# Performance work log

Measured on AMD Instinct MI355X. Metric: run time of the kernel, lower is better.

Reference implementation:

```python
import jax, jax.numpy as jnp
import numpy as np

N, DIN, D, H, L, S, E = 3072, 64, 128, 4, 2, 4, 49152
NEG = -2.0**32 + 1.0


def _layernorm(x, g, b, eps=1e-5):
    m = jnp.mean(x, axis=-1, keepdims=True)
    v = jnp.var(x, axis=-1, keepdims=True)
    return (x - m) * jax.lax.rsqrt(v + eps) * g + b


def setup_inputs() -> dict:
    key = jax.random.key(0)
    ks = jax.random.split(key, 24)
    w = lambda k, shp: (0.02 * jax.random.normal(k, shp)).astype(jnp.float32)
    inp = {
        "x": jax.random.normal(ks[0], (N, DIN), dtype=jnp.float32),
        "edge_index": jax.random.randint(ks[1], (2, E), 0, N, dtype=jnp.int64) if jax.config.jax_enable_x64 else jax.random.randint(ks[1], (2, E), 0, N).astype(jnp.int32),
        "shortest_path_len": jax.random.randint(ks[2], (N, N), 0, 11).astype(jnp.int32),
        "edge_feat": jax.random.normal(ks[3], (N, N, S), dtype=jnp.float32),
        # input projection
        "node_W": w(ks[4], (DIN, D)), "node_b": jnp.zeros((D,), jnp.float32),
        # centrality / spatial / edge encodings
        "deg_emb": w(ks[5], (N, D)),
        "sp_emb": w(ks[6], (11, 1)),
        "edge_W": w(ks[7], (S, S)), "edge_b": jnp.zeros((S,), jnp.float32),
        # per-layer stacked attention params
        "ln1_g": jnp.ones((L, D), jnp.float32), "ln1_b": jnp.zeros((L, D), jnp.float32),
        "Wq": w(ks[8], (L, H, D, D)), "bq": jnp.zeros((L, H, D), jnp.float32),
        "Wk": w(ks[9], (L, H, D, D)), "bk": jnp.zeros((L, H, D), jnp.float32),
        "Wv": w(ks[10], (L, H, D, D)), "bv": jnp.zeros((L, H, D), jnp.float32),
        "Wo": w(ks[11], (L, H * D, D)), "bo": jnp.zeros((L, D), jnp.float32),
        "ln2_g": jnp.ones((L, D), jnp.float32), "ln2_b": jnp.zeros((L, D), jnp.float32),
        "ff_W": w(ks[12], (L, D, D)), "ff_b": jnp.zeros((L, D), jnp.float32),
        # output projection
        "out_W": w(ks[13], (D, D)), "out_b": jnp.zeros((D,), jnp.float32),
    }
    return inp


def reference(x, edge_index, shortest_path_len, edge_feat,
              node_W, node_b, deg_emb, sp_emb, edge_W, edge_b,
              ln1_g, ln1_b, Wq, bq, Wk, bk, Wv, bv, Wo, bo,
              ln2_g, ln2_b, ff_W, ff_b, out_W, out_b):
    # padding mask from raw features
    mask_idx = (jnp.sum(x, axis=1) != 0).astype(x.dtype)            # [N]
    mask = mask_idx[:, None] * mask_idx[None, :]                    # [N,N]

    h = x @ node_W + node_b                                         # [N,D]
    # centrality: degree of edge destinations
    deg = jax.ops.segment_sum(jnp.ones((edge_index.shape[1],), jnp.int32),
                              edge_index[1], num_segments=N)        # [N]
    h = h + deg_emb[deg]

    spatial = sp_emb[shortest_path_len][..., 0]                     # [N,N]
    edge_m = (edge_feat @ edge_W + edge_b).mean(axis=-1)            # [N,N]
    bias = spatial + edge_m
    scale = 1.0 / jnp.sqrt(jnp.asarray(D, x.dtype))

    for l in range(L):
        x_ln = _layernorm(h, ln1_g[l], ln1_b[l])                    # [N,D]
        q = jnp.einsum('nd,hdk->hnk', x_ln, Wq[l]) + bq[l][:, None, :]
        k = jnp.einsum('nd,hdk->hnk', x_ln, Wk[l]) + bk[l][:, None, :]
        v = jnp.einsum('nd,hdk->hnk', x_ln, Wv[l]) + bv[l][:, None, :]
        a = jnp.einsum('hnk,hmk->hnm', q, k) * scale + bias[None]   # [H,N,N]
        a = jnp.where(mask[None] == 0, NEG, a)
        s = jax.nn.softmax(a, axis=-1)
        s = jnp.where(mask[None] == 0, 0.0, s)
        o = jnp.einsum('hnm,hmd->hnd', s, v)                        # [H,N,D]
        cat = jnp.transpose(o, (1, 0, 2)).reshape(N, H * D)         # [N,H*D]
        x_out = cat @ Wo[l] + bo[l] + h
        h = _layernorm(x_out, ln2_g[l], ln2_b[l]) @ ff_W[l] + ff_b[l] + x_out

    return h @ out_W + out_b
```

## Files before the change

### kernel.cpp

```cpp
#include <hip/hip_runtime.h>
#include <math.h>

static constexpr int N   = 3072;
static constexpr int DIN = 64;
static constexpr int D   = 128;
static constexpr int H   = 4;
static constexpr int E   = 49152;
#define NEGV  (-4294967295.0f)
#define SCALE (0.08838834764831845f)

typedef unsigned short u16;
typedef __attribute__((ext_vector_type(8))) short short8;
typedef __attribute__((ext_vector_type(4))) float f32x4;
typedef __attribute__((ext_vector_type(4))) unsigned short u16x4;

__device__ __forceinline__ u16 f2bf(float f){
  unsigned int u = __float_as_uint(f);
  u += 0x7fff + ((u >> 16) & 1);
  return (u16)(u >> 16);
}
__device__ __forceinline__ float bf2f(u16 u){
  return __uint_as_float(((unsigned int)u) << 16);
}

__global__ void k_zero_deg(int* __restrict__ deg){
  int i = blockIdx.x*blockDim.x + threadIdx.x;
  if(i < N) deg[i] = 0;
}

__global__ void k_deg(const int* __restrict__ ei, int* __restrict__ deg){
  int e = blockIdx.x*blockDim.x + threadIdx.x;
  if(e < E) atomicAdd(&deg[ei[E + e]], 1);
}

__global__ void k_h0(const float* __restrict__ x, const float* __restrict__ nodeW,
                     const float* __restrict__ nodeb, const float* __restrict__ degemb,
                     const int* __restrict__ deg, float* __restrict__ mask,
                     float* __restrict__ h){
  const int i = blockIdx.x, t = threadIdx.x;
  float xv = x[i*DIN + t];
  float s = xv;
  #pragma unroll
  for(int o=32;o;o>>=1) s += __shfl_xor(s, o);
  if(t == 0) mask[i] = (s != 0.0f) ? 1.0f : 0.0f;
  __shared__ float xr[DIN];
  xr[t] = xv;
  __syncthreads();
  int dg = deg[i]; dg = dg > N-1 ? N-1 : dg;
  float a0 = nodeb[t]      + degemb[dg*D + t];
  float a1 = nodeb[t + 64] + degemb[dg*D + t + 64];
  #pragma unroll
  for(int u=0; u<DIN; ++u){
    float xu = xr[u];
    a0 = fmaf(xu, nodeW[u*D + t],      a0);
    a1 = fmaf(xu, nodeW[u*D + t + 64], a1);
  }
  h[i*D + t]      = a0;
  h[i*D + t + 64] = a1;
}

__global__ void k_bias(const int* __restrict__ spl, const float* __restrict__ ef,
                       const float* __restrict__ spe, const float* __restrict__ eW,
                       const float* __restrict__ eb, const float* __restrict__ mask,
                       u16* __restrict__ biasm){
  int idx = blockIdx.x*blockDim.x + threadIdx.x;
  int i = idx / N, j = idx % N;
  float wm0 = (eW[0] + eW[1] + eW[2] + eW[3])  * 0.25f;
  float wm1 = (eW[4] + eW[5] + eW[6] + eW[7])  * 0.25f;
  float wm2 = (eW[8] + eW[9] + eW[10]+ eW[11]) * 0.25f;
  float wm3 = (eW[12]+ eW[13]+ eW[14]+ eW[15]) * 0.25f;
  float bm  = (eb[0] + eb[1] + eb[2] + eb[3])  * 0.25f;
  float4 e4 = reinterpret_cast<const float4*>(ef)[idx];
  float em = fmaf(e4.x, wm0, fmaf(e4.y, wm1, fmaf(e4.z, wm2, fmaf(e4.w, wm3, bm))));
  float b = spe[spl[idx]] + em;
  float mk = mask[i]*mask[j];
  biasm[idx] = f2bf((mk != 0.0f) ? b : NEGV);
}

__global__ void k_ln(const float* __restrict__ in, const float* __restrict__ g,
                     const float* __restrict__ b, float* __restrict__ out){
  const int w = threadIdx.x >> 6, lane = threadIdx.x & 63;
  const int row = blockIdx.x*4 + w;
  const float* r = in + row*D;
  float v0 = r[lane], v1 = r[lane + 64];
  float s = v0 + v1, sq = v0*v0 + v1*v1;
  #pragma unroll
  for(int o=32;o;o>>=1){ s += __shfl_xor(s, o); sq += __shfl_xor(sq, o); }
  float mean = s*(1.0f/128.0f);
  float var  = sq*(1.0f/128.0f) - mean*mean;
  float inv  = rsqrtf(var + 1e-5f);
  out[row*D + lane]      = (v0 - mean)*inv*g[lane]      + b[lane];
  out[row*D + lane + 64] = (v1 - mean)*inv*g[lane + 64] + b[lane + 64];
}

__global__ __launch_bounds__(256) void k_wt_all(const float* __restrict__ Wq, const float* __restrict__ Wk,
    const float* __restrict__ Wv, const float* __restrict__ ffW, const float* __restrict__ outW,
    u16* __restrict__ wt_qkv, u16* __restrict__ wt_ff, u16* __restrict__ wt_out){
  __shared__ float t[32][33];
  const int z = blockIdx.y;
  const float* src; u16* dst;
  if(z < 24){
    int l = z/12, r = z%12;
    const float* W = (r>>2)==0 ? Wq : (r>>2)==1 ? Wk : Wv;
    src = W + (size_t)(l*4 + (r&3))*16384;
    dst = wt_qkv + (size_t)z*16384;
  } else if(z < 26){
    src = ffW + (size_t)(z-24)*16384; dst = wt_ff + (size_t)(z-24)*16384;
  } else { src = outW; dst = wt_out; }
  const int ki = blockIdx.x & 3, ni = blockIdx.x >> 2;
  const int tid = threadIdx.x;
  #pragma unroll
  for(int i=0;i<4;i++){
    int idx = tid + i*256, r = idx>>5, c = idx&31;
    t[r][c] = src[(size_t)(ki*32+r)*128 + ni*32 + c];
  }
  __syncthreads();
  #pragma unroll
  for(int i=0;i<4;i++){
    int idx = tid + i*256, r = idx>>5, c = idx&31;
    dst[(size_t)(ni*32+r)*128 + ki*32 + c] = f2bf(t[c][r]);
  }
}

__global__ __launch_bounds__(256) void k_wt_wo(const float* __restrict__ Wo, u16* __restrict__ wt_wo){
  __shared__ float t[32][33];
  const int l = blockIdx.y;
  const float* src = Wo + (size_t)l*65536;
  u16* dst = wt_wo + (size_t)l*65536;
  const int ki = blockIdx.x & 15, ni = blockIdx.x >> 4;
  const int tid = threadIdx.x;
  #pragma unroll
  for(int i=0;i<4;i++){
    int idx = tid + i*256, r = idx>>5, c = idx&31;
    t[r][c] = src[(size_t)(ki*32+r)*128 + ni*32 + c];
  }
  __syncthreads();
  #pragma unroll
  for(int i=0;i<4;i++){
    int idx = tid + i*256, r = idx>>5, c = idx&31;
    dst[(size_t)(ni*32+r)*512 + ki*32 + c] = f2bf(t[c][r]);
  }
}

template<int K, bool RES, bool BF16OUT>
__device__ __forceinline__ void mgemm_body(const float* __restrict__ A, const u16* __restrict__ Bt,
                                           const float* __restrict__ bias, const float* __restrict__ res,
                                           void* __restrict__ Cv){
  __shared__ u16 As[64*128];
  __shared__ u16 Bs[128*128];
  const int tid = threadIdx.x, w = tid>>6, lane = tid&63;
  const int g4 = lane>>4, l16 = lane&15;
  const int m0 = blockIdx.x*64;
  const int srow = tid>>4, sch = tid&15;
  f32x4 acc[8];
  #pragma unroll
  for(int nt=0;nt<8;++nt) acc[nt] = (f32x4){0.f,0.f,0.f,0.f};
  for(int k0 = 0; k0 < K; k0 += 128){
    __syncthreads();
    #pragma unroll
    for(int it=0;it<4;++it){
      int row = it*16 + srow;
      const float4* ap = reinterpret_cast<const float4*>(A + (size_t)(m0+row)*K + k0 + sch*8);
      float4 x0 = ap[0], x1 = ap[1];
      u16x4 p0, p1;
      p0.x=f2bf(x0.x); p0.y=f2bf(x0.y); p0.z=f2bf(x0.z); p0.w=f2bf(x0.w);
      p1.x=f2bf(x1.x); p1.y=f2bf(x1.y); p1.z=f2bf(x1.z); p1.w=f2bf(x1.w);
      u16* dst = &As[row*128 + ((sch ^ (row&15))*8)];
      *reinterpret_cast<u16x4*>(dst)     = p0;
      *reinterpret_cast<u16x4*>(dst + 4) = p1;
    }
    #pragma unroll
    for(int it=0;it<8;++it){
      int row = it*16 + srow;
      short8 b = *reinterpret_cast<const short8*>(Bt + (size_t)row*K + k0 + sch*8);
      *reinterpret_cast<short8*>(&Bs[row*128 + ((sch ^ (row&15))*8)]) = b;
    }
    __syncthreads();
    __builtin_amdgcn_s_setprio(1);
    #pragma unroll
    for(int c=0;c<4;++c){
      short8 af = *reinterpret_cast<const short8*>(&As[(w*16+l16)*128 + (((c*4+g4) ^ l16)*8)]);
      #pragma unroll
      for(int nt=0;nt<8;++nt){
        short8 bf = *reinterpret_cast<const short8*>(&Bs[(nt*16+l16)*128 + (((c*4+g4) ^ l16)*8)]);
        acc[nt] = __builtin_amdgcn_mfma_f32_16x16x32_bf16(af, bf, acc[nt], 0, 0, 0);
      }
    }
    __builtin_amdgcn_s_setprio(0);
  }
  const int mrow = m0 + w*16 + g4*4;
  #pragma unroll
  for(int nt=0;nt<8;++nt){
    const int col = nt*16 + l16;
    float bi = bias[col];
    #pragma unroll
    for(int rg=0;rg<4;++rg){
      float v = acc[nt][rg] + bi;
      if(RES) v += res[(size_t)(mrow+rg)*128 + col];
      if(BF16OUT) ((u16*)Cv)[(size_t)(mrow+rg)*128 + col] = f2bf(v);
      else        ((float*)Cv)[(size_t)(mrow+rg)*128 + col] = v;
    }
  }
}

__global__ __launch_bounds__(256) void k_mqkv(const float* __restrict__ xln, const u16* __restrict__ wt_qkv,
    const float* __restrict__ bq, const float* __restrict__ bk, const float* __restrict__ bv,
    u16* __restrict__ q, u16* __restrict__ k, u16* __restrict__ v, int l){
  const int z = blockIdx.y, which = z>>2, head = z&3;
  const u16* Bt = wt_qkv + (size_t)(l*12 + z)*16384;
  const float* bb = (which==0 ? bq : which==1 ? bk : bv) + (l*H + head)*D;
  u16* out = (which==0 ? q : which==1 ? k : v) + (size_t)head*N*D;
  mgemm_body<128,false,true>(xln, Bt, bb, nullptr, out);
}

__global__ __launch_bounds__(256) void k_mwo(const float* __restrict__ ocat, const u16* __restrict__ wt_wo,
    const float* __restrict__ bo, const float* __restrict__ hres, float* __restrict__ xout, int l){
  mgemm_body<512,true,false>(ocat, wt_wo + (size_t)l*65536, bo + l*D, hres, xout);
}

__global__ __launch_bounds__(256) void k_mff(const float* __restrict__ xln, const u16* __restrict__ wt_ff,
    const float* __restrict__ ffb, const float* __restrict__ xout, float* __restrict__ h, int l){
  mgemm_body<128,true,false>(xln, wt_ff + (size_t)l*16384, ffb + l*D, xout, h);
}

__global__ __launch_bounds__(256) void k_mout(const float* __restrict__ h, const u16* __restrict__ wt_out,
    const float* __restrict__ outb, float* __restrict__ out){
  mgemm_body<128,false,false>(h, wt_out, outb, nullptr, out);
}

__global__ __launch_bounds__(256) void k_vt(const u16* __restrict__ vb, u16* __restrict__ vT){
  __shared__ u16 t[32][33];
  const int n0 = blockIdx.x*32, d0 = blockIdx.y*32, head = blockIdx.z;
  const int tid = threadIdx.x;
  #pragma unroll
  for(int i=0;i<4;i++){
    int idx = tid + i*256, r = idx >> 5, c = idx & 31;
    t[r][c] = vb[((size_t)head*N + n0 + r)*D + d0 + c];
  }
  __syncthreads();
  #pragma unroll
  for(int i=0;i<4;i++){
    int idx = tid + i*256, r = idx >> 5, c = idx & 31;
    vT[((size_t)head*D + d0 + r)*N + n0 + c] = t[c][r];
  }
}

__global__ __launch_bounds__(256) void k_attn(const u16* __restrict__ q, const u16* __restrict__ k,
                     const u16* __restrict__ vT, const u16* __restrict__ biasm,
                     float* __restrict__ opart, float* __restrict__ mpart, float* __restrict__ lpart,
                     int kvlen){
  const int tid  = threadIdx.x;
  const int w    = tid >> 6;
  const int lane = tid & 63;
  const int g4 = lane >> 4, l16 = lane & 15;
  const int head = blockIdx.y, sp = blockIdx.z;
  const int r0 = blockIdx.x*64 + w*16;
  __shared__ u16 Ks[64*128];
  __shared__ u16 Vs[64*128];
  __shared__ u16 P[4][16][40];

  const u16* qbase = q + ((size_t)head*N + r0)*D;
  short8 qf[4];
  #pragma unroll
  for(int c=0;c<4;c++)
    qf[c] = *reinterpret_cast<const short8*>(qbase + l16*D + c*32 + g4*8);

  f32x4 o[8];
  #pragma unroll
  for(int dt=0;dt<8;dt++) o[dt] = (f32x4){0.f,0.f,0.f,0.f};
  float m = -INFINITY, lsum = 0.0f;

  const u16* kh   = k  + (size_t)head*N*D;
  const u16* vTh  = vT + (size_t)head*D*N;
  const u16* brow = biasm + (size_t)(r0 + l16)*N;
  const int kv0 = sp*kvlen;

  const int krow = tid >> 4, kch = tid & 15;
  const int vrow = tid >> 3, vch = tid & 7;

  for(int j0 = kv0; j0 < kv0 + kvlen; j0 += 64){
    short8 kreg[4], vreg[4];
    #pragma unroll
    for(int it=0; it<4; ++it)
      kreg[it] = *reinterpret_cast<const short8*>(kh + (size_t)(j0 + it*16 + krow)*D + kch*8);
    #pragma unroll
    for(int it=0; it<4; ++it)
      vreg[it] = *reinterpret_cast<const short8*>(vTh + (size_t)(it*32 + vrow)*N + j0 + vch*8);
    u16x4 bb[4];
    #pragma unroll
    for(int z=0; z<4; ++z)
      bb[z] = *reinterpret_cast<const u16x4*>(brow + j0 + z*16 + g4*4);

    __syncthreads();
    #pragma unroll
    for(int it=0; it<4; ++it){
      int row = it*16 + krow;
      *reinterpret_cast<short8*>(&Ks[row*128 + ((kch ^ (row&15))*8)]) = kreg[it];
    }
    #pragma unroll
    for(int it=0; it<4; ++it){
      int d = it*32 + vrow;
      int row = d & 63, ch = ((d>>6)<<3) | vch;
      *reinterpret_cast<short8*>(&Vs[row*128 + ((ch ^ (row&15))*8)]) = vreg[it];
    }
    __syncthreads();

    #pragma unroll
    for(int ks=0; ks<2; ++ks){
      short8 kf[8];
      const int rowA = ks*32 + l16, rowB = rowA + 16;
      #pragma unroll
      for(int c=0;c<4;c++){
        kf[c]   = *reinterpret_cast<const short8*>(&Ks[rowA*128 + (((c*4+g4) ^ l16)*8)]);
        kf[4+c] = *reinterpret_cast<const short8*>(&Ks[rowB*128 + (((c*4+g4) ^ l16)*8)]);
      }
      f32x4 sA = (f32x4){0.f,0.f,0.f,0.f}, sB = sA;
      __builtin_amdgcn_s_setprio(1);
      #pragma unroll
      for(int c=0;c<4;c++){
        sA = __builtin_amdgcn_mfma_f32_16x16x32_bf16(kf[c],   qf[c], sA, 0, 0, 0);
        sB = __builtin_amdgcn_mfma_f32_16x16x32_bf16(kf[4+c], qf[c], sB, 0, 0, 0);
      }
      __builtin_amdgcn_s_setprio(0);
      u16x4 bA = bb[2*ks], bB = bb[2*ks+1];
      sA[0] = fmaf(sA[0], SCALE, bf2f(bA.x)); sA[1] = fmaf(sA[1], SCALE, bf2f(bA.y));
      sA[2] = fmaf(sA[2], SCALE, bf2f(bA.z)); sA[3] = fmaf(sA[3], SCALE, bf2f(bA.w));
      sB[0] = fmaf(sB[0], SCALE, bf2f(bB.x)); sB[1] = fmaf(sB[1], SCALE, bf2f(bB.y));
      sB[2] = fmaf(sB[2], SCALE, bf2f(bB.z)); sB[3] = fmaf(sB[3], SCALE, bf2f(bB.w));
      float pmax = fmaxf(fmaxf(fmaxf(sA[0],sA[1]), fmaxf(sA[2],sA[3])),
                         fmaxf(fmaxf(sB[0],sB[1]), fmaxf(sB[2],sB[3])));
      pmax = fmaxf(pmax, __shfl_xor(pmax, 16));
      pmax = fmaxf(pmax, __shfl_xor(pmax, 32));
      if(!__all(pmax - m <= 8.0f)){
        float mnew = fmaxf(m, pmax);
        float corr = __expf(m - mnew);
        lsum *= corr;
        float c0 = __shfl(corr, (lane & 48) | (g4*4 + 0));
        float c1 = __shfl(corr, (lane & 48) | (g4*4 + 1));
        float c2 = __shfl(corr, (lane & 48) | (g4*4 + 2));
        float c3 = __shfl(corr, (lane & 48) | (g4*4 + 3));
        #pragma unroll
        for(int dt=0;dt<8;dt++){
          o[dt][0] *= c0; o[dt][1] *= c1; o[dt][2] *= c2; o[dt][3] *= c3;
        }
        m = mnew;
      }
      f32x4 pA, pB;
      #pragma unroll
      for(int rg=0;rg<4;rg++){ pA[rg] = __expf(sA[rg] - m); pB[rg] = __expf(sB[rg] - m); }
      float ps = (pA[0]+pA[1]) + (pA[2]+pA[3]) + ((pB[0]+pB[1]) + (pB[2]+pB[3]));
      ps += __shfl_xor(ps, 16);
      ps += __shfl_xor(ps, 32);
      lsum += ps;
      u16x4 wa, wb;
      wa.x = f2bf(pA[0]); wa.y = f2bf(pA[1]); wa.z = f2bf(pA[2]); wa.w = f2bf(pA[3]);
      wb.x = f2bf(pB[0]); wb.y = f2bf(pB[1]); wb.z = f2bf(pB[2]); wb.w = f2bf(pB[3]);
      *reinterpret_cast<u16x4*>(&P[w][l16][g4*4])      = wa;
      *reinterpret_cast<u16x4*>(&P[w][l16][16 + g4*4]) = wb;
      short8 pf = *reinterpret_cast<const short8*>(&P[w][l16][g4*8]);
      __builtin_amdgcn_s_setprio(1);
      #pragma unroll
      for(int dt=0;dt<8;dt++){
        int d = dt*16 + l16;
        int row = d & 63;
        int ch  = ((dt>>2)<<3) | (ks<<2) | g4;
        short8 vf = *reinterpret_cast<const short8*>(&Vs[row*128 + ((ch ^ l16)*8)]);
        o[dt] = __builtin_amdgcn_mfma_f32_16x16x32_bf16(pf, vf, o[dt], 0, 0, 0);
      }
      __builtin_amdgcn_s_setprio(0);
    }
  }

  float* ob = opart + ((size_t)((sp*H + head)*N) + r0)*D;
  #pragma unroll
  for(int dt=0;dt<8;dt++){
    #pragma unroll
    for(int rg=0;rg<4;rg++)
      ob[(size_t)(g4*4+rg)*D + dt*16 + l16] = o[dt][rg];
  }
  if(g4 == 0){
    mpart[(size_t)(sp*H + head)*N + r0 + l16] = m;
    lpart[(size_t)(sp*H + head)*N + r0 + l16] = lsum;
  }
}

template<int S>
__global__ __launch_bounds__(256) void k_comb(const float* __restrict__ opart,
                      const float* __restrict__ mpart, const float* __restrict__ lpart,
                      const float* __restrict__ mask, float* __restrict__ ocat){
  int idx = blockIdx.x*256 + threadIdx.x;
  int d = idx & (D-1);
  int r = (idx >> 7) % N;
  int h = idx / (N*D);
  float mv[S], lv[S];
  float M = -INFINITY;
  #pragma unroll
  for(int s=0;s<S;s++){
    size_t p = (size_t)(s*H + h)*N + r;
    mv[s] = mpart[p]; lv[s] = lpart[p];
    M = fmaxf(M, mv[s]);
  }
  float denom = 0.f, val = 0.f;
  #pragma unroll
  for(int s=0;s<S;s++){
    size_t p = (size_t)(s*H + h)*N + r;
    float wgt = __expf(mv[s] - M);
    denom = fmaf(lv[s], wgt, denom);
    val   = fmaf(opart[p*D + d], wgt, val);
  }
  ocat[(size_t)r*(H*D) + h*D + d] = val * (mask[r] / denom);
}

extern "C" void kernel_launch(void* const* d_in, const int* in_sizes, int n_in,
                              void* d_out, int out_size, void* d_ws, size_t ws_size,
                              hipStream_t stream){
  const float* x      = (const float*)d_in[0];
  const int*   ei     = (const int*)  d_in[1];
  const int*   spl    = (const int*)  d_in[2];
  const float* ef     = (const float*)d_in[3];
  const float* nodeW  = (const float*)d_in[4];
  const float* nodeb  = (const float*)d_in[5];
  const float* degemb = (const float*)d_in[6];
  const float* spe    = (const float*)d_in[7];
  const float* eW     = (const float*)d_in[8];
  const float* eb     = (const float*)d_in[9];
  const float* ln1g   = (const float*)d_in[10];
  const float* ln1b   = (const float*)d_in[11];
  const float* Wq     = (const float*)d_in[12];
  const float* bq     = (const float*)d_in[13];
  const float* Wk     = (const float*)d_in[14];
  const float* bk     = (const float*)d_in[15];
  const float* Wv     = (const float*)d_in[16];
  const float* bv     = (const float*)d_in[17];
  const float* Wo     = (const float*)d_in[18];
  const float* bo     = (const float*)d_in[19];
  const float* ln2g   = (const float*)d_in[20];
  const float* ln2b   = (const float*)d_in[21];
  const float* ffW    = (const float*)d_in[22];
  const float* ffb    = (const float*)d_in[23];
  const float* outW   = (const float*)d_in[24];
  const float* outb   = (const float*)d_in[25];

  constexpr size_t WT_ELEMS = 24*16384 + 2*16384 + 16384 + 2*65536;
  auto needed = [](int s)->size_t{
    size_t fl = 8192 + 3*(size_t)N*D + (size_t)N*H*D;
    size_t bf = 4*(size_t)H*N*D + (size_t)N*N;
    size_t pf = (size_t)s*H*N*D + 2*(size_t)s*H*N;
    return fl*4 + bf*2 + pf*4 + WT_ELEMS*2;
  };
  int S = 2;
  if(needed(4) <= ws_size) S = 4;

  float* ws   = (float*)d_ws;
  int*   deg  = (int*)ws;
  float* mask = ws + 4096;
  float* h    = ws + 8192;
  float* xln  = h    + N*D;
  float* xout = xln  + N*D;
  float* ocat = xout + N*D;
  u16*   qb   = (u16*)(ocat + N*H*D);
  u16*   kb   = qb + (size_t)H*N*D;
  u16*   vb   = kb + (size_t)H*N*D;
  u16*   vT   = vb + (size_t)H*N*D;
  u16*   biasm= vT + (size_t)H*N*D;
  float* opart= (float*)(biasm + (size_t)N*N);
  float* mpart= opart + (size_t)S*H*N*D;
  float* lpart= mpart + (size_t)S*H*N;
  u16*   wt_qkv = (u16*)(lpart + (size_t)S*H*N);
  u16*   wt_ff  = wt_qkv + 24*16384;
  u16*   wt_out = wt_ff  + 2*16384;
  u16*   wt_wo  = wt_out + 16384;

  k_wt_all<<<dim3(16, 27), 256, 0, stream>>>(Wq, Wk, Wv, ffW, outW, wt_qkv, wt_ff, wt_out);
  k_wt_wo<<<dim3(64, 2), 256, 0, stream>>>(Wo, wt_wo);
  k_zero_deg<<<(N+255)/256, 256, 0, stream>>>(deg);
  k_deg<<<(E+255)/256, 256, 0, stream>>>(ei, deg);
  k_h0<<<N, 64, 0, stream>>>(x, nodeW, nodeb, degemb, deg, mask, h);
  k_bias<<<(N*N)/256, 256, 0, stream>>>(spl, ef, spe, eW, eb, mask, biasm);

  for(int l = 0; l < 2; ++l){
    k_ln<<<N/4, 256, 0, stream>>>(h, ln1g + l*D, ln1b + l*D, xln);
    k_mqkv<<<dim3(N/64, 12), 256, 0, stream>>>(xln, wt_qkv, bq, bk, bv, qb, kb, vb, l);
    k_vt<<<dim3(N/32, D/32, H), 256, 0, stream>>>(vb, vT);
    k_attn<<<dim3(N/64, H, S), 256, 0, stream>>>(qb, kb, vT, biasm, opart, mpart, lpart, N/S);
    if(S == 4) k_comb<4><<<(H*N*D)/256, 256, 0, stream>>>(opart, mpart, lpart, mask, ocat);
    else       k_comb<2><<<(H*N*D)/256, 256, 0, stream>>>(opart, mpart, lpart, mask, ocat);
    k_mwo<<<N/64, 256, 0, stream>>>(ocat, wt_wo, bo, h, xout, l);
    k_ln<<<N/4, 256, 0, stream>>>(xout, ln2g + l*D, ln2b + l*D, xln);
    k_mff<<<N/64, 256, 0, stream>>>(xln, wt_ff, ffb, xout, h, l);
  }
  k_mout<<<N/64, 256, 0, stream>>>(h, wt_out, outb, (float*)d_out);
}
```

Baseline: 236.5 us.

## Fuse layernorms, split-softmax combine and V transpose into neighboring GEMMs; prefetch attention tiles

```diff
diff --git a/kernel.cpp b/kernel.cpp
--- a/kernel.cpp
+++ b/kernel.cpp
@@ -35,8 +35,9 @@
 
 __global__ void k_h0(const float* __restrict__ x, const float* __restrict__ nodeW,
                      const float* __restrict__ nodeb, const float* __restrict__ degemb,
-                     const int* __restrict__ deg, float* __restrict__ mask,
-                     float* __restrict__ h){
+                     const int* __restrict__ deg, const float* __restrict__ g1,
+                     const float* __restrict__ b1, float* __restrict__ mask,
+                     float* __restrict__ h, float* __restrict__ xln){
   const int i = blockIdx.x, t = threadIdx.x;
   float xv = x[i*DIN + t];
   float s = xv;
@@ -57,6 +58,14 @@
   }
   h[i*D + t]      = a0;
   h[i*D + t + 64] = a1;
+  float s2 = a0 + a1, sq = a0*a0 + a1*a1;
+  #pragma unroll
+  for(int o=32;o;o>>=1){ s2 += __shfl_xor(s2, o); sq += __shfl_xor(sq, o); }
+  float mean = s2*(1.0f/128.0f);
+  float var  = sq*(1.0f/128.0f) - mean*mean;
+  float inv  = rsqrtf(var + 1e-5f);
+  xln[i*D + t]      = (a0 - mean)*inv*g1[t]      + b1[t];
+  xln[i*D + t + 64] = (a1 - mean)*inv*g1[t + 64] + b1[t + 64];
 }
 
 __global__ void k_bias(const int* __restrict__ spl, const float* __restrict__ ef,
@@ -77,22 +86,6 @@
   biasm[idx] = f2bf((mk != 0.0f) ? b : NEGV);
 }
 
-__global__ void k_ln(const float* __restrict__ in, const float* __restrict__ g,
-                     const float* __restrict__ b, float* __restrict__ out){
-  const int w = threadIdx.x >> 6, lane = threadIdx.x & 63;
-  const int row = blockIdx.x*4 + w;
-  const float* r = in + row*D;
-  float v0 = r[lane], v1 = r[lane + 64];
-  float s = v0 + v1, sq = v0*v0 + v1*v1;
-  #pragma unroll
-  for(int o=32;o;o>>=1){ s += __shfl_xor(s, o); sq += __shfl_xor(sq, o); }
-  float mean = s*(1.0f/128.0f);
-  float var  = sq*(1.0f/128.0f) - mean*mean;
-  float inv  = rsqrtf(var + 1e-5f);
-  out[row*D + lane]      = (v0 - mean)*inv*g[lane]      + b[lane];
-  out[row*D + lane + 64] = (v1 - mean)*inv*g[lane + 64] + b[lane + 64];
-}
-
 __global__ __launch_bounds__(256) void k_wt_all(const float* __restrict__ Wq, const float* __restrict__ Wk,
     const float* __restrict__ Wv, const float* __restrict__ ffW, const float* __restrict__ outW,
     u16* __restrict__ wt_qkv, u16* __restrict__ wt_ff, u16* __restrict__ wt_out){
@@ -142,10 +135,9 @@
   }
 }
 
-template<int K, bool RES, bool BF16OUT>
+template<int MODE>
 __device__ __forceinline__ void mgemm_body(const float* __restrict__ A, const u16* __restrict__ Bt,
-                                           const float* __restrict__ bias, const float* __restrict__ res,
-                                           void* __restrict__ Cv){
+                                           const float* __restrict__ bias, void* __restrict__ Cv){
   __shared__ u16 As[64*128];
   __shared__ u16 Bs[128*128];
   const int tid = threadIdx.x, w = tid>>6, lane = tid&63;
@@ -155,16 +147,120 @@
   f32x4 acc[8];
   #pragma unroll
   for(int nt=0;nt<8;++nt) acc[nt] = (f32x4){0.f,0.f,0.f,0.f};
-  for(int k0 = 0; k0 < K; k0 += 128){
+  #pragma unroll
+  for(int it=0;it<4;++it){
+    int row = it*16 + srow;
+    const float4* ap = reinterpret_cast<const float4*>(A + (size_t)(m0+row)*128 + sch*8);
+    float4 x0 = ap[0], x1 = ap[1];
+    u16x4 p0, p1;
+    p0.x=f2bf(x0.x); p0.y=f2bf(x0.y); p0.z=f2bf(x0.z); p0.w=f2bf(x0.w);
+    p1.x=f2bf(x1.x); p1.y=f2bf(x1.y); p1.z=f2bf(x1.z); p1.w=f2bf(x1.w);
+    u16* dst = &As[row*128 + ((sch ^ (row&15))*8)];
+    *reinterpret_cast<u16x4*>(dst)     = p0;
+    *reinterpret_cast<u16x4*>(dst + 4) = p1;
+  }
+  #pragma unroll
+  for(int it=0;it<8;++it){
+    int row = it*16 + srow;
+    short8 b = *reinterpret_cast<const short8*>(Bt + (size_t)row*128 + sch*8);
+    *reinterpret_cast<short8*>(&Bs[row*128 + ((sch ^ (row&15))*8)]) = b;
+  }
+  __syncthreads();
+  __builtin_amdgcn_s_setprio(1);
+  #pragma unroll
+  for(int c=0;c<4;++c){
+    short8 af = *reinterpret_cast<const short8*>(&As[(w*16+l16)*128 + (((c*4+g4) ^ l16)*8)]);
+    #pragma unroll
+    for(int nt=0;nt<8;++nt){
+      short8 bf = *reinterpret_cast<const short8*>(&Bs[(nt*16+l16)*128 + (((c*4+g4) ^ l16)*8)]);
+      acc[nt] = __builtin_amdgcn_mfma_f32_16x16x32_bf16(af, bf, acc[nt], 0, 0, 0);
+    }
+  }
+  __builtin_amdgcn_s_setprio(0);
+  const int mrow = m0 + w*16 + g4*4;
+  #pragma unroll
+  for(int nt=0;nt<8;++nt){
+    const int col = nt*16 + l16;
+    float bi = bias[col];
+    if(MODE == 2){
+      u16x4 t;
+      t.x = f2bf(acc[nt][0] + bi); t.y = f2bf(acc[nt][1] + bi);
+      t.z = f2bf(acc[nt][2] + bi); t.w = f2bf(acc[nt][3] + bi);
+      *reinterpret_cast<u16x4*>((u16*)Cv + (size_t)col*N + mrow) = t;
+    } else {
+      #pragma unroll
+      for(int rg=0;rg<4;++rg){
+        float v = acc[nt][rg] + bi;
+        if(MODE == 1) ((u16*)Cv)[(size_t)(mrow+rg)*128 + col] = f2bf(v);
+        else          ((float*)Cv)[(size_t)(mrow+rg)*128 + col] = v;
+      }
+    }
+  }
+}
+
+__global__ __launch_bounds__(256) void k_mqkv(const float* __restrict__ xln, const u16* __restrict__ wt_qkv,
+    const float* __restrict__ bq, const float* __restrict__ bk, const float* __restrict__ bv,
+    u16* __restrict__ q, u16* __restrict__ k, u16* __restrict__ vT, int l){
+  const int z = blockIdx.y, which = z>>2, head = z&3;
+  const u16* Bt = wt_qkv + (size_t)(l*12 + z)*16384;
+  if(which == 0)      mgemm_body<1>(xln, Bt, bq + (l*H+head)*D, q  + (size_t)head*N*D);
+  else if(which == 1) mgemm_body<1>(xln, Bt, bk + (l*H+head)*D, k  + (size_t)head*N*D);
+  else                mgemm_body<2>(xln, Bt, bv + (l*H+head)*D, vT + (size_t)head*N*D);
+}
+
+__global__ __launch_bounds__(256) void k_mout(const float* __restrict__ h, const u16* __restrict__ wt_out,
+    const float* __restrict__ outb, float* __restrict__ out){
+  mgemm_body<0>(h, wt_out, outb, out);
+}
+
+template<int S>
+__global__ __launch_bounds__(256) void k_mwo(const float* __restrict__ opart, const float* __restrict__ mpart,
+    const float* __restrict__ lpart, const float* __restrict__ mask, const u16* __restrict__ wt,
+    const float* __restrict__ bo, const float* __restrict__ hres,
+    float* __restrict__ xout, float* __restrict__ xln,
+    const float* __restrict__ g2, const float* __restrict__ b2){
+  __shared__ u16 As[64*128];
+  __shared__ u16 Bs[128*128];
+  const int tid = threadIdx.x, w = tid>>6, lane = tid&63;
+  const int g4 = lane>>4, l16 = lane&15;
+  const int m0 = blockIdx.x*64;
+  const int srow = tid>>4, sch = tid&15;
+  f32x4 acc[8];
+  #pragma unroll
+  for(int nt=0;nt<8;++nt) acc[nt] = (f32x4){0.f,0.f,0.f,0.f};
+  for(int k0 = 0; k0 < 512; k0 += 128){
+    const int hh = k0 >> 7;
     __syncthreads();
     #pragma unroll
     for(int it=0;it<4;++it){
       int row = it*16 + srow;
-      const float4* ap = reinterpret_cast<const float4*>(A + (size_t)(m0+row)*K + k0 + sch*8);
-      float4 x0 = ap[0], x1 = ap[1];
+      int grow = m0 + row;
+      float w_[S]; float M = -INFINITY; float mv[S], lv[S];
+      #pragma unroll
+      for(int s=0;s<S;++s){
+        mv[s] = mpart[(size_t)(s*H + hh)*N + grow];
+        lv[s] = lpart[(size_t)(s*H + hh)*N + grow];
+        M = fmaxf(M, mv[s]);
+      }
+      float denom = 0.f;
+      #pragma unroll
+      for(int s=0;s<S;++s){ w_[s] = __expf(mv[s] - M); denom = fmaf(lv[s], w_[s], denom); }
+      float scale = mask[grow] / denom;
+      const int d = sch*8;
+      float4 v0 = make_float4(0,0,0,0), v1 = make_float4(0,0,0,0);
+      #pragma unroll
+      for(int s=0;s<S;++s){
+        const float4* op = reinterpret_cast<const float4*>(
+            opart + ((size_t)(s*H + hh)*N + grow)*D + d);
+        float4 a = op[0], b = op[1];
+        v0.x = fmaf(a.x, w_[s], v0.x); v0.y = fmaf(a.y, w_[s], v0.y);
+        v0.z = fmaf(a.z, w_[s], v0.z); v0.w = fmaf(a.w, w_[s], v0.w);
+        v1.x = fmaf(b.x, w_[s], v1.x); v1.y = fmaf(b.y, w_[s], v1.y);
+        v1.z = fmaf(b.z, w_[s], v1.z); v1.w = fmaf(b.w, w_[s], v1.w);
+      }
       u16x4 p0, p1;
-      p0.x=f2bf(x0.x); p0.y=f2bf(x0.y); p0.z=f2bf(x0.z); p0.w=f2bf(x0.w);
-      p1.x=f2bf(x1.x); p1.y=f2bf(x1.y); p1.z=f2bf(x1.z); p1.w=f2bf(x1.w);
+      p0.x=f2bf(v0.x*scale); p0.y=f2bf(v0.y*scale); p0.z=f2bf(v0.z*scale); p0.w=f2bf(v0.w*scale);
+      p1.x=f2bf(v1.x*scale); p1.y=f2bf(v1.y*scale); p1.z=f2bf(v1.z*scale); p1.w=f2bf(v1.w*scale);
       u16* dst = &As[row*128 + ((sch ^ (row&15))*8)];
       *reinterpret_cast<u16x4*>(dst)     = p0;
       *reinterpret_cast<u16x4*>(dst + 4) = p1;
@@ -172,7 +268,7 @@
     #pragma unroll
     for(int it=0;it<8;++it){
       int row = it*16 + srow;
-      short8 b = *reinterpret_cast<const short8*>(Bt + (size_t)row*K + k0 + sch*8);
+      short8 b = *reinterpret_cast<const short8*>(wt + (size_t)row*512 + k0 + sch*8);
       *reinterpret_cast<short8*>(&Bs[row*128 + ((sch ^ (row&15))*8)]) = b;
     }
     __syncthreads();
@@ -189,59 +285,127 @@
     __builtin_amdgcn_s_setprio(0);
   }
   const int mrow = m0 + w*16 + g4*4;
+  float s_[4] = {0,0,0,0}, q_[4] = {0,0,0,0};
   #pragma unroll
   for(int nt=0;nt<8;++nt){
     const int col = nt*16 + l16;
-    float bi = bias[col];
+    float bi = bo[col];
     #pragma unroll
     for(int rg=0;rg<4;++rg){
-      float v = acc[nt][rg] + bi;
-      if(RES) v += res[(size_t)(mrow+rg)*128 + col];
-      if(BF16OUT) ((u16*)Cv)[(size_t)(mrow+rg)*128 + col] = f2bf(v);
-      else        ((float*)Cv)[(size_t)(mrow+rg)*128 + col] = v;
-    }
-  }
-}
-
-__global__ __launch_bounds__(256) void k_mqkv(const float* __restrict__ xln, const u16* __restrict__ wt_qkv,
-    const float* __restrict__ bq, const float* __restrict__ bk, const float* __restrict__ bv,
-    u16* __restrict__ q, u16* __restrict__ k, u16* __restrict__ v, int l){
-  const int z = blockIdx.y, which = z>>2, head = z&3;
-  const u16* Bt = wt_qkv + (size_t)(l*12 + z)*16384;
-  const float* bb = (which==0 ? bq : which==1 ? bk : bv) + (l*H + head)*D;
-  u16* out = (which==0 ? q : which==1 ? k : v) + (size_t)head*N*D;
-  mgemm_body<128,false,true>(xln, Bt, bb, nullptr, out);
-}
-
-__global__ __launch_bounds__(256) void k_mwo(const float* __restrict__ ocat, const u16* __restrict__ wt_wo,
-    const float* __restrict__ bo, const float* __restrict__ hres, float* __restrict__ xout, int l){
-  mgemm_body<512,true,false>(ocat, wt_wo + (size_t)l*65536, bo + l*D, hres, xout);
-}
-
-__global__ __launch_bounds__(256) void k_mff(const float* __restrict__ xln, const u16* __restrict__ wt_ff,
-    const float* __restrict__ ffb, const float* __restrict__ xout, float* __restrict__ h, int l){
-  mgemm_body<128,true,false>(xln, wt_ff + (size_t)l*16384, ffb + l*D, xout, h);
-}
-
-__global__ __launch_bounds__(256) void k_mout(const float* __restrict__ h, const u16* __restrict__ wt_out,
-    const float* __restrict__ outb, float* __restrict__ out){
-  mgemm_body<128,false,false>(h, wt_out, outb, nullptr, out);
-}
-
-__global__ __launch_bounds__(256) void k_vt(const u16* __restrict__ vb, u16* __restrict__ vT){
-  __shared__ u16 t[32][33];
-  const int n0 = blockIdx.x*32, d0 = blockIdx.y*32, head = blockIdx.z;
-  const int tid = threadIdx.x;
-  #pragma unroll
-  for(int i=0;i<4;i++){
-    int idx = tid + i*256, r = idx >> 5, c = idx & 31;
-    t[r][c] = vb[((size_t)head*N + n0 + r)*D + d0 + c];
+      float v = acc[nt][rg] + bi + hres[(size_t)(mrow+rg)*128 + col];
+      acc[nt][rg] = v;
+      s_[rg] += v; q_[rg] = fmaf(v, v, q_[rg]);
+    }
+  }
+  #pragma unroll
+  for(int o=1;o<16;o<<=1){
+    #pragma unroll
+    for(int rg=0;rg<4;++rg){ s_[rg] += __shfl_xor(s_[rg], o); q_[rg] += __shfl_xor(q_[rg], o); }
+  }
+  float mean[4], inv[4];
+  #pragma unroll
+  for(int rg=0;rg<4;++rg){
+    mean[rg] = s_[rg]*(1.0f/128.0f);
+    float var = q_[rg]*(1.0f/128.0f) - mean[rg]*mean[rg];
+    inv[rg] = rsqrtf(var + 1e-5f);
+  }
+  #pragma unroll
+  for(int nt=0;nt<8;++nt){
+    const int col = nt*16 + l16;
+    float gg = g2[col], bb = b2[col];
+    #pragma unroll
+    for(int rg=0;rg<4;++rg){
+      float v = acc[nt][rg];
+      xout[(size_t)(mrow+rg)*128 + col] = v;
+      xln [(size_t)(mrow+rg)*128 + col] = (v - mean[rg])*inv[rg]*gg + bb;
+    }
+  }
+}
+
+__global__ __launch_bounds__(256) void k_mff(const float* __restrict__ xlnin, const u16* __restrict__ wt,
+    const float* __restrict__ ffb, const float* __restrict__ res, float* __restrict__ hout,
+    float* __restrict__ xlnout, const float* __restrict__ g1n, const float* __restrict__ b1n,
+    int write_ln){
+  __shared__ u16 As[64*128];
+  __shared__ u16 Bs[128*128];
+  const int tid = threadIdx.x, w = tid>>6, lane = tid&63;
+  const int g4 = lane>>4, l16 = lane&15;
+  const int m0 = blockIdx.x*64;
+  const int srow = tid>>4, sch = tid&15;
+  f32x4 acc[8];
+  #pragma unroll
+  for(int nt=0;nt<8;++nt) acc[nt] = (f32x4){0.f,0.f,0.f,0.f};
+  #pragma unroll
+  for(int it=0;it<4;++it){
+    int row = it*16 + srow;
+    const float4* ap = reinterpret_cast<const float4*>(xlnin + (size_t)(m0+row)*128 + sch*8);
+    float4 x0 = ap[0], x1 = ap[1];
+    u16x4 p0, p1;
+    p0.x=f2bf(x0.x); p0.y=f2bf(x0.y); p0.z=f2bf(x0.z); p0.w=f2bf(x0.w);
+    p1.x=f2bf(x1.x); p1.y=f2bf(x1.y); p1.z=f2bf(x1.z); p1.w=f2bf(x1.w);
+    u16* dst = &As[row*128 + ((sch ^ (row&15))*8)];
+    *reinterpret_cast<u16x4*>(dst)     = p0;
+    *reinterpret_cast<u16x4*>(dst + 4) = p1;
+  }
+  #pragma unroll
+  for(int it=0;it<8;++it){
+    int row = it*16 + srow;
+    short8 b = *reinterpret_cast<const short8*>(wt + (size_t)row*128 + sch*8);
+    *reinterpret_cast<short8*>(&Bs[row*128 + ((sch ^ (row&15))*8)]) = b;
   }
   __syncthreads();
-  #pragma unroll
-  for(int i=0;i<4;i++){
-    int idx = tid + i*256, r = idx >> 5, c = idx & 31;
-    vT[((size_t)head*D + d0 + r)*N + n0 + c] = t[c][r];
+  __builtin_amdgcn_s_setprio(1);
+  #pragma unroll
+  for(int c=0;c<4;++c){
+    short8 af = *reinterpret_cast<const short8*>(&As[(w*16+l16)*128 + (((c*4+g4) ^ l16)*8)]);
+    #pragma unroll
+    for(int nt=0;nt<8;++nt){
+      short8 bf = *reinterpret_cast<const short8*>(&Bs[(nt*16+l16)*128 + (((c*4+g4) ^ l16)*8)]);
+      acc[nt] = __builtin_amdgcn_mfma_f32_16x16x32_bf16(af, bf, acc[nt], 0, 0, 0);
+    }
+  }
+  __builtin_amdgcn_s_setprio(0);
+  const int mrow = m0 + w*16 + g4*4;
+  float s_[4] = {0,0,0,0}, q_[4] = {0,0,0,0};
+  #pragma unroll
+  for(int nt=0;nt<8;++nt){
+    const int col = nt*16 + l16;
+    float bi = ffb[col];
+    #pragma unroll
+    for(int rg=0;rg<4;++rg){
+      float v = acc[nt][rg] + bi + res[(size_t)(mrow+rg)*128 + col];
+      acc[nt][rg] = v;
+      s_[rg] += v; q_[rg] = fmaf(v, v, q_[rg]);
+    }
+  }
+  #pragma unroll
+  for(int nt=0;nt<8;++nt){
+    const int col = nt*16 + l16;
+    #pragma unroll
+    for(int rg=0;rg<4;++rg)
+      hout[(size_t)(mrow+rg)*128 + col] = acc[nt][rg];
+  }
+  if(write_ln){
+    #pragma unroll
+    for(int o=1;o<16;o<<=1){
+      #pragma unroll
+      for(int rg=0;rg<4;++rg){ s_[rg] += __shfl_xor(s_[rg], o); q_[rg] += __shfl_xor(q_[rg], o); }
+    }
+    #pragma unroll
+    for(int rg=0;rg<4;++rg){
+      float mean = s_[rg]*(1.0f/128.0f);
+      float var  = q_[rg]*(1.0f/128.0f) - mean*mean;
+      float inv  = rsqrtf(var + 1e-5f);
+      s_[rg] = mean; q_[rg] = inv;
+    }
+    #pragma unroll
+    for(int nt=0;nt<8;++nt){
+      const int col = nt*16 + l16;
+      float gg = g1n[col], bb = b1n[col];
+      #pragma unroll
+      for(int rg=0;rg<4;++rg)
+        xlnout[(size_t)(mrow+rg)*128 + col] = (acc[nt][rg] - s_[rg])*q_[rg]*gg + bb;
+    }
   }
 }
 
@@ -278,19 +442,19 @@
   const int krow = tid >> 4, kch = tid & 15;
   const int vrow = tid >> 3, vch = tid & 7;
 
+  short8 kreg[4], vreg[4]; u16x4 bb[4];
+  #pragma unroll
+  for(int it=0; it<4; ++it)
+    kreg[it] = *reinterpret_cast<const short8*>(kh + (size_t)(kv0 + it*16 + krow)*D + kch*8);
+  #pragma unroll
+  for(int it=0; it<4; ++it)
+    vreg[it] = *reinterpret_cast<const short8*>(vTh + (size_t)(it*32 + vrow)*N + kv0 + vch*8);
+  #pragma unroll
+  for(int z=0; z<4; ++z)
+    bb[z] = *reinterpret_cast<const u16x4*>(brow + kv0 + z*16 + g4*4);
+
   for(int j0 = kv0; j0 < kv0 + kvlen; j0 += 64){
-    short8 kreg[4], vreg[4];
-    #pragma unroll
-    for(int it=0; it<4; ++it)
-      kreg[it] = *reinterpret_cast<const short8*>(kh + (size_t)(j0 + it*16 + krow)*D + kch*8);
-    #pragma unroll
-    for(int it=0; it<4; ++it)
-      vreg[it] = *reinterpret_cast<const short8*>(vTh + (size_t)(it*32 + vrow)*N + j0 + vch*8);
-    u16x4 bb[4];
-    #pragma unroll
-    for(int z=0; z<4; ++z)
-      bb[z] = *reinterpret_cast<const u16x4*>(brow + j0 + z*16 + g4*4);
-
+    const int jn = (j0 + 64 < kv0 + kvlen) ? j0 + 64 : kv0;
     __syncthreads();
     #pragma unroll
     for(int it=0; it<4; ++it){
@@ -304,6 +468,17 @@
       *reinterpret_cast<short8*>(&Vs[row*128 + ((ch ^ (row&15))*8)]) = vreg[it];
     }
     __syncthreads();
+
+    short8 kreg2[4], vreg2[4]; u16x4 bb2[4];
+    #pragma unroll
+    for(int it=0; it<4; ++it)
+      kreg2[it] = *reinterpret_cast<const short8*>(kh + (size_t)(jn + it*16 + krow)*D + kch*8);
+    #pragma unroll
+    for(int it=0; it<4; ++it)
+      vreg2[it] = *reinterpret_cast<const short8*>(vTh + (size_t)(it*32 + vrow)*N + jn + vch*8);
+    #pragma unroll
+    for(int z=0; z<4; ++z)
+      bb2[z] = *reinterpret_cast<const u16x4*>(brow + jn + z*16 + g4*4);
 
     #pragma unroll
     for(int ks=0; ks<2; ++ks){
@@ -369,6 +544,10 @@
       }
       __builtin_amdgcn_s_setprio(0);
     }
+    #pragma unroll
+    for(int it=0; it<4; ++it){ kreg[it] = kreg2[it]; vreg[it] = vreg2[it]; }
+    #pragma unroll
+    for(int z=0; z<4; ++z) bb[z] = bb2[z];
   }
 
   float* ob = opart + ((size_t)((sp*H + head)*N) + r0)*D;
@@ -382,33 +561,6 @@
     mpart[(size_t)(sp*H + head)*N + r0 + l16] = m;
     lpart[(size_t)(sp*H + head)*N + r0 + l16] = lsum;
   }
-}
-
-template<int S>
-__global__ __launch_bounds__(256) void k_comb(const float* __restrict__ opart,
-                      const float* __restrict__ mpart, const float* __restrict__ lpart,
-                      const float* __restrict__ mask, float* __restrict__ ocat){
-  int idx = blockIdx.x*256 + threadIdx.x;
-  int d = idx & (D-1);
-  int r = (idx >> 7) % N;
-  int h = idx / (N*D);
-  float mv[S], lv[S];
-  float M = -INFINITY;
-  #pragma unroll
-  for(int s=0;s<S;s++){
-    size_t p = (size_t)(s*H + h)*N + r;
-    mv[s] = mpart[p]; lv[s] = lpart[p];
-    M = fmaxf(M, mv[s]);
-  }
-  float denom = 0.f, val = 0.f;
-  #pragma unroll
-  for(int s=0;s<S;s++){
-    size_t p = (size_t)(s*H + h)*N + r;
-    float wgt = __expf(mv[s] - M);
-    denom = fmaf(lv[s], wgt, denom);
-    val   = fmaf(opart[p*D + d], wgt, val);
-  }
-  ocat[(size_t)r*(H*D) + h*D + d] = val * (mask[r] / denom);
 }
 
 extern "C" void kernel_launch(void* const* d_in, const int* in_sizes, int n_in,
@@ -443,8 +595,8 @@
 
   constexpr size_t WT_ELEMS = 24*16384 + 2*16384 + 16384 + 2*65536;
   auto needed = [](int s)->size_t{
-    size_t fl = 8192 + 3*(size_t)N*D + (size_t)N*H*D;
-    size_t bf = 4*(size_t)H*N*D + (size_t)N*N;
+    size_t fl = 8192 + 3*(size_t)N*D;
+    size_t bf = 3*(size_t)H*N*D + (size_t)N*N;
     size_t pf = (size_t)s*H*N*D + 2*(size_t)s*H*N;
     return fl*4 + bf*2 + pf*4 + WT_ELEMS*2;
   };
@@ -457,12 +609,10 @@
   float* h    = ws + 8192;
   float* xln  = h    + N*D;
   float* xout = xln  + N*D;
-  float* ocat = xout + N*D;
-  u16*   qb   = (u16*)(ocat + N*H*D);
+  u16*   qb   = (u16*)(xout + N*D);
   u16*   kb   = qb + (size_t)H*N*D;
-  u16*   vb   = kb + (size_t)H*N*D;
-  u16*   vT   = vb + (size_t)H*N*D;
-  u16*   biasm= vT + (size_t)H*N*D;
+  u16*   vTb  = kb + (size_t)H*N*D;
+  u16*   biasm= vTb + (size_t)H*N*D;
   float* opart= (float*)(biasm + (size_t)N*N);
   float* mpart= opart + (size_t)S*H*N*D;
   float* lpart= mpart + (size_t)S*H*N;
@@ -475,19 +625,20 @@
   k_wt_wo<<<dim3(64, 2), 256, 0, stream>>>(Wo, wt_wo);
   k_zero_deg<<<(N+255)/256, 256, 0, stream>>>(deg);
   k_deg<<<(E+255)/256, 256, 0, stream>>>(ei, deg);
-  k_h0<<<N, 64, 0, stream>>>(x, nodeW, nodeb, degemb, deg, mask, h);
+  k_h0<<<N, 64, 0, stream>>>(x, nodeW, nodeb, degemb, deg, ln1g, ln1b, mask, h, xln);
   k_bias<<<(N*N)/256, 256, 0, stream>>>(spl, ef, spe, eW, eb, mask, biasm);
 
   for(int l = 0; l < 2; ++l){
-    k_ln<<<N/4, 256, 0, stream>>>(h, ln1g + l*D, ln1b + l*D, xln);
-    k_mqkv<<<dim3(N/64, 12), 256, 0, stream>>>(xln, wt_qkv, bq, bk, bv, qb, kb, vb, l);
-    k_vt<<<dim3(N/32, D/32, H), 256, 0, stream>>>(vb, vT);
-    k_attn<<<dim3(N/64, H, S), 256, 0, stream>>>(qb, kb, vT, biasm, opart, mpart, lpart, N/S);
-    if(S == 4) k_comb<4><<<(H*N*D)/256, 256, 0, stream>>>(opart, mpart, lpart, mask, ocat);
-    else       k_comb<2><<<(H*N*D)/256, 256, 0, stream>>>(opart, mpart, lpart, mask, ocat);
-    k_mwo<<<N/64, 256, 0, stream>>>(ocat, wt_wo, bo, h, xout, l);
-    k_ln<<<N/4, 256, 0, stream>>>(xout, ln2g + l*D, ln2b + l*D, xln);
-    k_mff<<<N/64, 256, 0, stream>>>(xln, wt_ff, ffb, xout, h, l);
+    k_mqkv<<<dim3(N/64, 12), 256, 0, stream>>>(xln, wt_qkv, bq, bk, bv, qb, kb, vTb, l);
+    k_attn<<<dim3(N/64, H, S), 256, 0, stream>>>(qb, kb, vTb, biasm, opart, mpart, lpart, N/S);
+    if(S == 4)
+      k_mwo<4><<<N/64, 256, 0, stream>>>(opart, mpart, lpart, mask, wt_wo + (size_t)l*65536,
+                                         bo + l*D, h, xout, xln, ln2g + l*D, ln2b + l*D);
+    else
+      k_mwo<2><<<N/64, 256, 0, stream>>>(opart, mpart, lpart, mask, wt_wo + (size_t)l*65536,
+                                         bo + l*D, h, xout, xln, ln2g + l*D, ln2b + l*D);
+    k_mff<<<N/64, 256, 0, stream>>>(xln, wt_ff + (size_t)l*16384, ffb + l*D, xout, h, xln,
+                                    ln1g + (l==0 ? D : 0), ln1b + (l==0 ? D : 0), l==0 ? 1 : 0);
   }
   k_mout<<<N/64, 256, 0, stream>>>(h, wt_out, outb, (float*)d_out);
 }
```

Result: slower. 265.3 us (+12.2%).
